# Performance work log

Measured on AMD Instinct MI355X. Metric: run time of the kernel, lower is better.

## Reference

```python
import jax, jax.numpy as jnp
import numpy as np

NZ = 1024       # opts.nz (== NH so layer-0 input weights stack with other layers)
NH = 1024       # opts.nh
NSTATE = 64     # opts.n_state
NLAYERS = 4
MAX_PRIM_LEN = 100
T = MAX_PRIM_LEN + 1   # max_unroll=True runs exactly max_prim_len+1 steps
P_BIAS = 1.0           # opts.dec_p_bias


def setup_inputs() -> dict:
    key = jax.random.key(0)
    ks = jax.random.split(key, 9)
    s_ih = 1.0 / np.sqrt(NH)
    u = lambda k, shape: jax.random.uniform(k, shape, jnp.float32, -s_ih, s_ih)
    return {
        "z": jax.random.normal(ks[0], (1, NZ), jnp.float32),
        # torch LSTM params, gate order (i, f, g, o); layer0 input dim == NZ == NH
        "Wih": u(ks[1], (NLAYERS, 4 * NH, NH)),
        "Whh": u(ks[2], (NLAYERS, 4 * NH, NH)),
        "bih": u(ks[3], (NLAYERS, 4 * NH)),
        "bhh": u(ks[4], (NLAYERS, 4 * NH)),
        "Ws": u(ks[5], (NSTATE, NH)),
        "bs": u(ks[6], (NSTATE,)),
        "Wp": u(ks[7], (2, NH)),
        "bp": u(ks[8], (2,)),
    }


def reference(z, Wih, Whh, bih, bhh, Ws, bs, Wp, bp):
    z0 = z.reshape(-1)  # (NZ,)
    zeros = jnp.zeros_like(z0)

    def step(carry, i):
        h, c = carry                      # each (NLAYERS, NH)
        x = jnp.where(i == 0, z0, zeros)  # input is z at t=0, zeros after
        hs, cs = [], []
        inp = x
        for l in range(NLAYERS):
            gates = Wih[l] @ inp + bih[l] + Whh[l] @ h[l] + bhh[l]
            gi, gf, gg, go = jnp.split(gates, 4)
            cl = jax.nn.sigmoid(gf) * c[l] + jax.nn.sigmoid(gi) * jnp.tanh(gg)
            hl = jax.nn.sigmoid(go) * jnp.tanh(cl)
            hs.append(hl)
            cs.append(cl)
            inp = hl
        o = inp                            # top-layer output, (NH,)
        s = Ws @ o + bs                    # state head, (NSTATE,)
        logits = (Wp @ o + bp).at[0].add(P_BIAS)
        p = jax.nn.softmax(logits)         # (2,)
        last = i == T - 1                  # torch: t > max_prim_len -> force [0,1]
        p = jnp.where(last, jnp.array([0.0, 1.0], p.dtype), p)
        samp = jnp.where(last, 1, 0).astype(jnp.int64)  # max_unroll forces 0 until last
        return (jnp.stack(hs), jnp.stack(cs)), (s, p, samp)

    h0 = jnp.zeros((NLAYERS, NH), z.dtype)
    _, (states, probs, samples) = jax.lax.scan(step, (h0, h0), jnp.arange(T))
    return states[:, None, :], probs[:, None, :], samples[:, None]
```

## Files before the change

### kernel.cpp

```cpp
#include <hip/hip_runtime.h>


#define TT    101
#define NBLK  256
#define NHEAD 65
#define NTH   512
#define NREP  8
#define SLAB_U32 512

#define HB16_BYTES (4 * TT * NREP * SLAB_U32 * 4)

#define OUT_PROBS 6464
#define OUT_SAMP  6666

typedef _Float16 h2 __attribute__((ext_vector_type(2)));

__device__ __forceinline__ h2 mkh2(float a, float b) {
    h2 r; r.x = (_Float16)a; r.y = (_Float16)b; return r;
}

#if __has_builtin(__builtin_amdgcn_fdot2)
__device__ __forceinline__ float fdot2(h2 a, h2 b, float c) {
    return __builtin_amdgcn_fdot2(a, b, c, false);
}
#else
__device__ __forceinline__ float fdot2(h2 a, h2 b, float c) {
    return fmaf((float)a.x, (float)b.x, fmaf((float)a.y, (float)b.y, c));
}
#endif

__device__ __forceinline__ uint4 load16_bypass(const uint4* p) {
    uint4 r;
    asm volatile("global_load_dwordx4 %0, %1, off sc0 sc1\n\ts_waitcnt vmcnt(0)"
                 : "=v"(r) : "v"(p) : "memory");
    return r;
}
__device__ __forceinline__ void store4_bypass(unsigned* p, unsigned v) {
    asm volatile("global_store_dword %0, %1, off sc0 sc1" :: "v"(p), "v"(v) : "memory");
}

__device__ __forceinline__ uint4 poll16(const uint4* p) {
    uint4 r = load16_bypass(p);
    while (r.x == 0xFFFFFFFFu || r.y == 0xFFFFFFFFu ||
           r.z == 0xFFFFFFFFu || r.w == 0xFFFFFFFFu) {
        __builtin_amdgcn_s_sleep(1);
        r = load16_bypass(p);
    }
    return r;
}

__device__ __forceinline__ float2 unpack(unsigned u) {
    h2 p = __builtin_bit_cast(h2, u);
    return make_float2((float)p.x, (float)p.y);
}

__global__ __launch_bounds__(NTH, 2) void lstm_kernel(
    const float* __restrict__ z,
    const float* __restrict__ Wih, const float* __restrict__ Whh,
    const float* __restrict__ bih, const float* __restrict__ bhh,
    const float* __restrict__ Ws,  const float* __restrict__ bs,
    const float* __restrict__ Wp,  const float* __restrict__ bp,
    unsigned* __restrict__ hb16, float* __restrict__ out)
{
    const int tid  = threadIdx.x;
    const int wv   = tid >> 6;
    const int lane = tid & 63;

    if (blockIdx.x >= NBLK) {
        if (wv != 0) return;
        const int hb  = blockIdx.x - NBLK;
        const int rep = hb & (NREP - 1);
        if (hb < 64) {
            float wr[16];
            #pragma unroll
            for (int k = 0; k < 16; ++k) wr[k] = Ws[(hb << 10) + (lane << 4) + k];
            const float bsv = bs[hb];
            for (int th = 0; th < TT; ++th) {
                const uint4* slab = (const uint4*)(hb16 + (size_t)((3 * TT + th) * NREP + rep) * SLAB_U32);
                const uint4 r0 = poll16(slab + 2 * lane);
                const uint4 r1 = poll16(slab + 2 * lane + 1);
                const unsigned u8[8] = {r0.x, r0.y, r0.z, r0.w, r1.x, r1.y, r1.z, r1.w};
                float a = 0.f;
                #pragma unroll
                for (int j = 0; j < 8; ++j) {
                    const float2 p = unpack(u8[j]);
                    a = fmaf(wr[2 * j], p.x, a);
                    a = fmaf(wr[2 * j + 1], p.y, a);
                }
                #pragma unroll
                for (int off = 1; off < 64; off <<= 1) a += __shfl_xor(a, off);
                if (lane == 0) out[th * 64 + hb] = a + bsv;
            }
        } else {
            float w0[16], w1[16];
            #pragma unroll
            for (int k = 0; k < 16; ++k) {
                w0[k] = Wp[(lane << 4) + k];
                w1[k] = Wp[1024 + (lane << 4) + k];
            }
            const float bp0 = bp[0], bp1 = bp[1];
            for (int th = 0; th < TT; ++th) {
                const uint4* slab = (const uint4*)(hb16 + (size_t)((3 * TT + th) * NREP + rep) * SLAB_U32);
                const uint4 r0 = poll16(slab + 2 * lane);
                const uint4 r1 = poll16(slab + 2 * lane + 1);
                const unsigned u8[8] = {r0.x, r0.y, r0.z, r0.w, r1.x, r1.y, r1.z, r1.w};
                float a0 = 0.f, a1 = 0.f;
                #pragma unroll
                for (int j = 0; j < 8; ++j) {
                    const float2 p = unpack(u8[j]);
                    a0 = fmaf(w0[2 * j], p.x, a0); a0 = fmaf(w0[2 * j + 1], p.y, a0);
                    a1 = fmaf(w1[2 * j], p.x, a1); a1 = fmaf(w1[2 * j + 1], p.y, a1);
                }
                #pragma unroll
                for (int off = 1; off < 64; off <<= 1) { a0 += __shfl_xor(a0, off); a1 += __shfl_xor(a1, off); }
                if (lane == 0) {
                    float p0, p1;
                    if (th == TT - 1) { p0 = 0.f; p1 = 1.f; }
                    else {
                        const float l0 = a0 + bp0 + 1.0f;
                        const float l1 = a1 + bp1;
                        const float m  = fmaxf(l0, l1);
                        const float e0 = expf(l0 - m), e1 = expf(l1 - m);
                        const float inv = 1.f / (e0 + e1);
                        p0 = e0 * inv; p1 = e1 * inv;
                    }
                    out[OUT_PROBS + 2 * th]     = p0;
                    out[OUT_PROBS + 2 * th + 1] = p1;
                    out[OUT_SAMP + th] = (th == TT - 1) ? 1.0f : 0.0f;
                }
            }
        }
        return;
    }

    const int l   = blockIdx.x >> 6;
    const int gb  = blockIdx.x & 63;
    const int uA  = (gb << 4) + (wv << 1);
    const int rep = gb & (NREP - 1);

    __shared__ __align__(16) h2 vh[1024];

    h2 w[8][16];
    #pragma unroll
    for (int r = 0; r < 8; ++r) {
        const int u = (r < 4) ? uA : (uA + 1);
        const int g = r & 3;
        const size_t row = ((size_t)((l << 12) + (g << 10) + u)) << 10;
        #pragma unroll
        for (int k = 0; k < 8; ++k) {
            const float2 fh = *(const float2*)(Whh + row + (size_t)(((k << 6) + lane) << 1));
            w[r][k] = mkh2(fh.x, fh.y);
            const float2 fi = *(const float2*)(Wih + row + (size_t)(((k << 6) + lane) << 1));
            w[r][8 + k] = mkh2(fi.x, fi.y);
        }
    }

    float bA[4], bB[4];
    #pragma unroll
    for (int g = 0; g < 4; ++g) {
        const int iA = (l << 12) + (g << 10) + uA;
        bA[g] = bih[iA] + bhh[iA];
        bB[g] = bih[iA + 1] + bhh[iA + 1];
    }

    float cst = 0.f;

    #pragma unroll 1
    for (int t = 0; t < TT; ++t) {
        const bool full = (l > 0) || (t == 0);

        if (tid < 128) {
            if (t == 0) {
                *(uint4*)&vh[tid << 2] = make_uint4(0, 0, 0, 0);
            } else {
                const uint4* slab = (const uint4*)(hb16 + (size_t)((l * TT + (t - 1)) * NREP + rep) * SLAB_U32);
                *(uint4*)&vh[tid << 2] = poll16(slab + tid);
            }
        } else if (tid < 256) {
            const int j = tid - 128;
            if (l > 0) {
                const uint4* slab = (const uint4*)(hb16 + (size_t)(((l - 1) * TT + t) * NREP + rep) * SLAB_U32);
                *(uint4*)&vh[512 + (j << 2)] = poll16(slab + j);
            } else if (t == 0) {
                const float4 f0 = *(const float4*)(z + (j << 3));
                const float4 f1 = *(const float4*)(z + (j << 3) + 4);
                h2 tmp[4] = {mkh2(f0.x, f0.y), mkh2(f0.z, f0.w),
                             mkh2(f1.x, f1.y), mkh2(f1.z, f1.w)};
                *(uint4*)&vh[512 + (j << 2)] = *(uint4*)tmp;
            }
        }
        __syncthreads();

        float acc[8] = {0.f, 0.f, 0.f, 0.f, 0.f, 0.f, 0.f, 0.f};
        #pragma unroll
        for (int k = 0; k < 8; ++k) {
            const h2 v2 = vh[(k << 6) + lane];
            #pragma unroll
            for (int r = 0; r < 8; ++r) acc[r] = fdot2(w[r][k], v2, acc[r]);
        }
        if (full) {
            #pragma unroll
            for (int k = 0; k < 8; ++k) {
                const h2 v2 = vh[512 + (k << 6) + lane];
                #pragma unroll
                for (int r = 0; r < 8; ++r) acc[r] = fdot2(w[r][8 + k], v2, acc[r]);
            }
        }
        #pragma unroll
        for (int off = 1; off < 64; off <<= 1) {
            #pragma unroll
            for (int r = 0; r < 8; ++r) acc[r] += __shfl_xor(acc[r], off);
        }

        float hv = 0.f;
        if (lane < 2) {
            float s0, s1, s2, s3;
            if (lane == 0) { s0 = acc[0] + bA[0]; s1 = acc[1] + bA[1]; s2 = acc[2] + bA[2]; s3 = acc[3] + bA[3]; }
            else           { s0 = acc[4] + bB[0]; s1 = acc[5] + bB[1]; s2 = acc[6] + bB[2]; s3 = acc[7] + bB[3]; }
            const float si = 1.f / (1.f + expf(-s0));
            const float sf = 1.f / (1.f + expf(-s1));
            const float so = 1.f / (1.f + expf(-s3));
            cst = fmaf(sf, cst, si * tanhf(s2));
            hv  = so * tanhf(cst);
        }
        const float hB = __shfl(hv, 1);
        if (lane == 0) {
            const unsigned packed = __builtin_bit_cast(unsigned, mkh2(hv, hB));
            unsigned* base = hb16 + (size_t)(l * TT + t) * NREP * SLAB_U32 + (gb << 3) + wv;
            #pragma unroll
            for (int r = 0; r < NREP; ++r) store4_bypass(base + r * SLAB_U32, packed);
        }
        __syncthreads();
    }
}

extern "C" void kernel_launch(void* const* d_in, const int* in_sizes, int n_in,
                              void* d_out, int out_size, void* d_ws, size_t ws_size,
                              hipStream_t stream)
{
    const float* z   = (const float*)d_in[0];
    const float* Wih = (const float*)d_in[1];
    const float* Whh = (const float*)d_in[2];
    const float* bih = (const float*)d_in[3];
    const float* bhh = (const float*)d_in[4];
    const float* Ws  = (const float*)d_in[5];
    const float* bs  = (const float*)d_in[6];
    const float* Wp  = (const float*)d_in[7];
    const float* bp  = (const float*)d_in[8];
    float* out = (float*)d_out;

    unsigned* hb16 = (unsigned*)d_ws;

    hipMemsetAsync(hb16, 0xFF, HB16_BYTES, stream);
    lstm_kernel<<<NBLK + NHEAD, NTH, 0, stream>>>(z, Wih, Whh, bih, bhh,
                                                  Ws, bs, Wp, bp, hb16, out);
}
```

Baseline: 566.1 us.

## Fold output heads into LSTM blocks, use DPP reductions and batched slab stores

Removes the 65 separate head blocks. The state and probability head dot products now run inside wave 6 of existing LSTM blocks, opportunistically polling the top-layer slabs a few steps behind and draining any remainder after the main loop. Wave reductions switch from shuffle-xor to DPP row operations with a readlane, and every lane computes the gate nonlinearities. The 8 hidden-state replicas are written by one wave through an LDS staging buffer instead of 8 serial stores from lane 0 of each wave. Slab replica selection is staggered per wave, and weights load as float4. The fused heads may add work to the critical path of the host blocks.

Measured after the change: 512.4 us. 9.5% less time.

```diff
diff --git a/kernel.cpp b/kernel.cpp
--- a/kernel.cpp
+++ b/kernel.cpp
@@ -3,21 +3,23 @@
 
 #define TT    101
 #define NBLK  256
-#define NHEAD 65
 #define NTH   512
 #define NREP  8
 #define SLAB_U32 512
-
 #define HB16_BYTES (4 * TT * NREP * SLAB_U32 * 4)
-
 #define OUT_PROBS 6464
 #define OUT_SAMP  6666
+#define SENT 0xFFFFFFFFu
 
 typedef _Float16 h2 __attribute__((ext_vector_type(2)));
 
 __device__ __forceinline__ h2 mkh2(float a, float b) {
     h2 r; r.x = (_Float16)a; r.y = (_Float16)b; return r;
 }
+__device__ __forceinline__ unsigned pack2(float a, float b) {
+    return __builtin_bit_cast(unsigned, mkh2(a, b));
+}
+__device__ __forceinline__ h2 as_h2(unsigned u) { return __builtin_bit_cast(h2, u); }
 
 #if __has_builtin(__builtin_amdgcn_fdot2)
 __device__ __forceinline__ float fdot2(h2 a, h2 b, float c) {
@@ -38,21 +40,33 @@
 __device__ __forceinline__ void store4_bypass(unsigned* p, unsigned v) {
     asm volatile("global_store_dword %0, %1, off sc0 sc1" :: "v"(p), "v"(v) : "memory");
 }
-
 __device__ __forceinline__ uint4 poll16(const uint4* p) {
     uint4 r = load16_bypass(p);
-    while (r.x == 0xFFFFFFFFu || r.y == 0xFFFFFFFFu ||
-           r.z == 0xFFFFFFFFu || r.w == 0xFFFFFFFFu) {
+    while (r.x == SENT || r.y == SENT || r.z == SENT || r.w == SENT) {
         __builtin_amdgcn_s_sleep(1);
         r = load16_bypass(p);
     }
     return r;
 }
 
-__device__ __forceinline__ float2 unpack(unsigned u) {
-    h2 p = __builtin_bit_cast(h2, u);
-    return make_float2((float)p.x, (float)p.y);
-}
+__device__ __forceinline__ float wave_sum(float x) {
+    int v;
+    v = __builtin_amdgcn_update_dpp(0, __builtin_bit_cast(int, x), 0x111, 0xf, 0xf, false);
+    x += __builtin_bit_cast(float, v);
+    v = __builtin_amdgcn_update_dpp(0, __builtin_bit_cast(int, x), 0x112, 0xf, 0xf, false);
+    x += __builtin_bit_cast(float, v);
+    v = __builtin_amdgcn_update_dpp(0, __builtin_bit_cast(int, x), 0x114, 0xf, 0xe, false);
+    x += __builtin_bit_cast(float, v);
+    v = __builtin_amdgcn_update_dpp(0, __builtin_bit_cast(int, x), 0x118, 0xf, 0xc, false);
+    x += __builtin_bit_cast(float, v);
+    v = __builtin_amdgcn_update_dpp(0, __builtin_bit_cast(int, x), 0x142, 0xa, 0xf, false);
+    x += __builtin_bit_cast(float, v);
+    v = __builtin_amdgcn_update_dpp(0, __builtin_bit_cast(int, x), 0x143, 0xc, 0xf, false);
+    x += __builtin_bit_cast(float, v);
+    return __builtin_bit_cast(float, __builtin_amdgcn_readlane(__builtin_bit_cast(int, x), 63));
+}
+
+__device__ __forceinline__ float sigm(float x) { return 1.f / (1.f + expf(-x)); }
 
 __global__ __launch_bounds__(NTH, 2) void lstm_kernel(
     const float* __restrict__ z,
@@ -65,60 +79,208 @@
     const int tid  = threadIdx.x;
     const int wv   = tid >> 6;
     const int lane = tid & 63;
-
-    if (blockIdx.x >= NBLK) {
-        if (wv != 0) return;
-        const int hb  = blockIdx.x - NBLK;
-        const int rep = hb & (NREP - 1);
-        if (hb < 64) {
-            float wr[16];
+    const int l    = blockIdx.x >> 6;
+    const int gb   = blockIdx.x & 63;
+    const int uA   = (gb << 4) + (wv << 1);
+
+    __shared__ __align__(16) uint4 vh4[256];
+    __shared__ unsigned hout[8];
+
+    h2 w[8][16];
+    #pragma unroll
+    for (int r = 0; r < 8; ++r) {
+        const int u = uA + (r >> 2);
+        const int g = r & 3;
+        const size_t row = ((size_t)((l << 12) + (g << 10) + u)) << 10;
+        const float4* pa = (const float4*)(Whh + row + (lane << 3));
+        const float4* pb = (const float4*)(Whh + row + 512 + (lane << 3));
+        const float4* pc = (const float4*)(Wih + row + (lane << 3));
+        const float4* pd = (const float4*)(Wih + row + 512 + (lane << 3));
+        float4 f;
+        f = pa[0]; w[r][0]  = mkh2(f.x, f.y); w[r][1]  = mkh2(f.z, f.w);
+        f = pa[1]; w[r][2]  = mkh2(f.x, f.y); w[r][3]  = mkh2(f.z, f.w);
+        f = pb[0]; w[r][4]  = mkh2(f.x, f.y); w[r][5]  = mkh2(f.z, f.w);
+        f = pb[1]; w[r][6]  = mkh2(f.x, f.y); w[r][7]  = mkh2(f.z, f.w);
+        f = pc[0]; w[r][8]  = mkh2(f.x, f.y); w[r][9]  = mkh2(f.z, f.w);
+        f = pc[1]; w[r][10] = mkh2(f.x, f.y); w[r][11] = mkh2(f.z, f.w);
+        f = pd[0]; w[r][12] = mkh2(f.x, f.y); w[r][13] = mkh2(f.z, f.w);
+        f = pd[1]; w[r][14] = mkh2(f.x, f.y); w[r][15] = mkh2(f.z, f.w);
+    }
+
+    float bA[4], bB[4];
+    #pragma unroll
+    for (int g = 0; g < 4; ++g) {
+        const int iA = (l << 12) + (g << 10) + uA;
+        bA[g] = bih[iA] + bhh[iA];
+        bB[g] = bih[iA + 1] + bhh[iA + 1];
+    }
+
+    const bool role_states = (l == 0 && wv == 6);
+    const bool role_probs  = (l == 1 && gb == 0 && wv == 6);
+    float hw0[16], hw1[16], hb0 = 0.f, hb1 = 0.f;
+    if (role_states) {
+        #pragma unroll
+        for (int k = 0; k < 16; ++k) hw0[k] = Ws[(gb << 10) + (lane << 4) + k];
+        hb0 = bs[gb];
+    } else if (role_probs) {
+        #pragma unroll
+        for (int k = 0; k < 16; ++k) {
+            hw0[k] = Wp[(lane << 4) + k];
+            hw1[k] = Wp[1024 + (lane << 4) + k];
+        }
+        hb0 = bp[0]; hb1 = bp[1];
+    }
+    int th = 0;
+
+    float cstA = 0.f, cstB = 0.f;
+
+    #pragma unroll 1
+    for (int t = 0; t < TT; ++t) {
+        const bool full = (l > 0) || (t == 0);
+        const int rep = (gb + wv) & (NREP - 1);
+
+        if (wv < 2) {
+            const int c = (wv << 6) + lane;
+            if (t == 0) vh4[c] = make_uint4(0, 0, 0, 0);
+            else {
+                const uint4* slab = (const uint4*)(hb16 + (size_t)((l * TT + t - 1) * NREP + rep) * SLAB_U32);
+                vh4[c] = poll16(slab + c);
+            }
+        } else if (wv < 4) {
+            const int c = ((wv - 2) << 6) + lane;
+            if (l > 0) {
+                const uint4* slab = (const uint4*)(hb16 + (size_t)(((l - 1) * TT + t) * NREP + rep) * SLAB_U32);
+                vh4[128 + c] = poll16(slab + c);
+            } else if (t == 0) {
+                const float4 f0 = *(const float4*)(z + (c << 3));
+                const float4 f1 = *(const float4*)(z + (c << 3) + 4);
+                vh4[128 + c] = make_uint4(pack2(f0.x, f0.y), pack2(f0.z, f0.w),
+                                          pack2(f1.x, f1.y), pack2(f1.z, f1.w));
+            }
+        }
+        __syncthreads();
+
+        float acc[8] = {0.f, 0.f, 0.f, 0.f, 0.f, 0.f, 0.f, 0.f};
+        {
+            const uint4 A1 = vh4[lane];
+            const uint4 A2 = vh4[64 + lane];
+            const unsigned a8[8] = {A1.x, A1.y, A1.z, A1.w, A2.x, A2.y, A2.z, A2.w};
             #pragma unroll
-            for (int k = 0; k < 16; ++k) wr[k] = Ws[(hb << 10) + (lane << 4) + k];
-            const float bsv = bs[hb];
-            for (int th = 0; th < TT; ++th) {
-                const uint4* slab = (const uint4*)(hb16 + (size_t)((3 * TT + th) * NREP + rep) * SLAB_U32);
-                const uint4 r0 = poll16(slab + 2 * lane);
-                const uint4 r1 = poll16(slab + 2 * lane + 1);
+            for (int k = 0; k < 8; ++k) {
+                const h2 v2 = as_h2(a8[k]);
+                #pragma unroll
+                for (int r = 0; r < 8; ++r) acc[r] = fdot2(w[r][k], v2, acc[r]);
+            }
+            if (full) {
+                const uint4 B1 = vh4[128 + lane];
+                const uint4 B2 = vh4[192 + lane];
+                const unsigned b8[8] = {B1.x, B1.y, B1.z, B1.w, B2.x, B2.y, B2.z, B2.w};
+                #pragma unroll
+                for (int k = 0; k < 8; ++k) {
+                    const h2 v2 = as_h2(b8[k]);
+                    #pragma unroll
+                    for (int r = 0; r < 8; ++r) acc[r] = fdot2(w[r][8 + k], v2, acc[r]);
+                }
+            }
+        }
+
+        float tot[8];
+        #pragma unroll
+        for (int r = 0; r < 8; ++r) tot[r] = wave_sum(acc[r]);
+
+        cstA = fmaf(sigm(tot[1] + bA[1]), cstA, sigm(tot[0] + bA[0]) * tanhf(tot[2] + bA[2]));
+        cstB = fmaf(sigm(tot[5] + bB[1]), cstB, sigm(tot[4] + bB[0]) * tanhf(tot[6] + bB[2]));
+        const float hA = sigm(tot[3] + bA[3]) * tanhf(cstA);
+        const float hB = sigm(tot[7] + bB[3]) * tanhf(cstB);
+        if (lane == 0) hout[wv] = pack2(hA, hB);
+        __syncthreads();
+
+        if (wv == 7) {
+            const unsigned val = hout[lane & 7];
+            unsigned* addr = hb16 + (size_t)(l * TT + t) * NREP * SLAB_U32
+                           + (size_t)(lane >> 3) * SLAB_U32 + (gb << 3) + (lane & 7);
+            store4_bypass(addr, val);
+        } else if ((role_states || role_probs) && th < TT && th <= t - 3) {
+            const int hrep = (gb + th) & (NREP - 1);
+            const uint4* slab3 = (const uint4*)(hb16 + (size_t)((3 * TT + th) * NREP + hrep) * SLAB_U32);
+            const uint4 r0 = load16_bypass(slab3 + (lane << 1));
+            const uint4 r1 = load16_bypass(slab3 + (lane << 1) + 1);
+            const bool ok = !(r0.x == SENT || r0.y == SENT || r0.z == SENT || r0.w == SENT ||
+                              r1.x == SENT || r1.y == SENT || r1.z == SENT || r1.w == SENT);
+            if (__ballot(ok) == ~0ull) {
                 const unsigned u8[8] = {r0.x, r0.y, r0.z, r0.w, r1.x, r1.y, r1.z, r1.w};
+                if (role_states) {
+                    float a = 0.f;
+                    #pragma unroll
+                    for (int j = 0; j < 8; ++j) {
+                        const h2 p = as_h2(u8[j]);
+                        a = fmaf(hw0[2 * j], (float)p.x, a);
+                        a = fmaf(hw0[2 * j + 1], (float)p.y, a);
+                    }
+                    const float tots = wave_sum(a);
+                    if (lane == 0) out[th * 64 + gb] = tots + hb0;
+                } else {
+                    float a0 = 0.f, a1 = 0.f;
+                    #pragma unroll
+                    for (int j = 0; j < 8; ++j) {
+                        const h2 p = as_h2(u8[j]);
+                        a0 = fmaf(hw0[2 * j], (float)p.x, a0); a0 = fmaf(hw0[2 * j + 1], (float)p.y, a0);
+                        a1 = fmaf(hw1[2 * j], (float)p.x, a1); a1 = fmaf(hw1[2 * j + 1], (float)p.y, a1);
+                    }
+                    const float t0 = wave_sum(a0), t1 = wave_sum(a1);
+                    if (lane == 0) {
+                        float p0, p1;
+                        if (th == TT - 1) { p0 = 0.f; p1 = 1.f; }
+                        else {
+                            const float l0 = t0 + hb0 + 1.0f;
+                            const float l1 = t1 + hb1;
+                            const float m  = fmaxf(l0, l1);
+                            const float e0 = expf(l0 - m), e1 = expf(l1 - m);
+                            const float inv = 1.f / (e0 + e1);
+                            p0 = e0 * inv; p1 = e1 * inv;
+                        }
+                        out[OUT_PROBS + 2 * th]     = p0;
+                        out[OUT_PROBS + 2 * th + 1] = p1;
+                        out[OUT_SAMP + th] = (th == TT - 1) ? 1.0f : 0.0f;
+                    }
+                }
+                ++th;
+            }
+        }
+    }
+
+    if (role_states || role_probs) {
+        while (th < TT) {
+            const int hrep = (gb + th) & (NREP - 1);
+            const uint4* slab3 = (const uint4*)(hb16 + (size_t)((3 * TT + th) * NREP + hrep) * SLAB_U32);
+            const uint4 r0 = poll16(slab3 + (lane << 1));
+            const uint4 r1 = poll16(slab3 + (lane << 1) + 1);
+            const unsigned u8[8] = {r0.x, r0.y, r0.z, r0.w, r1.x, r1.y, r1.z, r1.w};
+            if (role_states) {
                 float a = 0.f;
                 #pragma unroll
                 for (int j = 0; j < 8; ++j) {
-                    const float2 p = unpack(u8[j]);
-                    a = fmaf(wr[2 * j], p.x, a);
-                    a = fmaf(wr[2 * j + 1], p.y, a);
-                }
-                #pragma unroll
-                for (int off = 1; off < 64; off <<= 1) a += __shfl_xor(a, off);
-                if (lane == 0) out[th * 64 + hb] = a + bsv;
-            }
-        } else {
-            float w0[16], w1[16];
-            #pragma unroll
-            for (int k = 0; k < 16; ++k) {
-                w0[k] = Wp[(lane << 4) + k];
-                w1[k] = Wp[1024 + (lane << 4) + k];
-            }
-            const float bp0 = bp[0], bp1 = bp[1];
-            for (int th = 0; th < TT; ++th) {
-                const uint4* slab = (const uint4*)(hb16 + (size_t)((3 * TT + th) * NREP + rep) * SLAB_U32);
-                const uint4 r0 = poll16(slab + 2 * lane);
-                const uint4 r1 = poll16(slab + 2 * lane + 1);
-                const unsigned u8[8] = {r0.x, r0.y, r0.z, r0.w, r1.x, r1.y, r1.z, r1.w};
+                    const h2 p = as_h2(u8[j]);
+                    a = fmaf(hw0[2 * j], (float)p.x, a);
+                    a = fmaf(hw0[2 * j + 1], (float)p.y, a);
+                }
+                const float tots = wave_sum(a);
+                if (lane == 0) out[th * 64 + gb] = tots + hb0;
+            } else {
                 float a0 = 0.f, a1 = 0.f;
                 #pragma unroll
                 for (int j = 0; j < 8; ++j) {
-                    const float2 p = unpack(u8[j]);
-                    a0 = fmaf(w0[2 * j], p.x, a0); a0 = fmaf(w0[2 * j + 1], p.y, a0);
-                    a1 = fmaf(w1[2 * j], p.x, a1); a1 = fmaf(w1[2 * j + 1], p.y, a1);
-                }
-                #pragma unroll
-                for (int off = 1; off < 64; off <<= 1) { a0 += __shfl_xor(a0, off); a1 += __shfl_xor(a1, off); }
+                    const h2 p = as_h2(u8[j]);
+                    a0 = fmaf(hw0[2 * j], (float)p.x, a0); a0 = fmaf(hw0[2 * j + 1], (float)p.y, a0);
+                    a1 = fmaf(hw1[2 * j], (float)p.x, a1); a1 = fmaf(hw1[2 * j + 1], (float)p.y, a1);
+                }
+                const float t0 = wave_sum(a0), t1 = wave_sum(a1);
                 if (lane == 0) {
                     float p0, p1;
                     if (th == TT - 1) { p0 = 0.f; p1 = 1.f; }
                     else {
-                        const float l0 = a0 + bp0 + 1.0f;
-                        const float l1 = a1 + bp1;
+                        const float l0 = t0 + hb0 + 1.0f;
+                        const float l1 = t1 + hb1;
                         const float m  = fmaxf(l0, l1);
                         const float e0 = expf(l0 - m), e1 = expf(l1 - m);
                         const float inv = 1.f / (e0 + e1);
@@ -129,108 +291,8 @@
                     out[OUT_SAMP + th] = (th == TT - 1) ? 1.0f : 0.0f;
                 }
             }
-        }
-        return;
-    }
-
-    const int l   = blockIdx.x >> 6;
-    const int gb  = blockIdx.x & 63;
-    const int uA  = (gb << 4) + (wv << 1);
-    const int rep = gb & (NREP - 1);
-
-    __shared__ __align__(16) h2 vh[1024];
-
-    h2 w[8][16];
-    #pragma unroll
-    for (int r = 0; r < 8; ++r) {
-        const int u = (r < 4) ? uA : (uA + 1);
-        const int g = r & 3;
-        const size_t row = ((size_t)((l << 12) + (g << 10) + u)) << 10;
-        #pragma unroll
-        for (int k = 0; k < 8; ++k) {
-            const float2 fh = *(const float2*)(Whh + row + (size_t)(((k << 6) + lane) << 1));
-            w[r][k] = mkh2(fh.x, fh.y);
-            const float2 fi = *(const float2*)(Wih + row + (size_t)(((k << 6) + lane) << 1));
-            w[r][8 + k] = mkh2(fi.x, fi.y);
-        }
-    }
-
-    float bA[4], bB[4];
-    #pragma unroll
-    for (int g = 0; g < 4; ++g) {
-        const int iA = (l << 12) + (g << 10) + uA;
-        bA[g] = bih[iA] + bhh[iA];
-        bB[g] = bih[iA + 1] + bhh[iA + 1];
-    }
-
-    float cst = 0.f;
-
-    #pragma unroll 1
-    for (int t = 0; t < TT; ++t) {
-        const bool full = (l > 0) || (t == 0);
-
-        if (tid < 128) {
-            if (t == 0) {
-                *(uint4*)&vh[tid << 2] = make_uint4(0, 0, 0, 0);
-            } else {
-                const uint4* slab = (const uint4*)(hb16 + (size_t)((l * TT + (t - 1)) * NREP + rep) * SLAB_U32);
-                *(uint4*)&vh[tid << 2] = poll16(slab + tid);
-            }
-        } else if (tid < 256) {
-            const int j = tid - 128;
-            if (l > 0) {
-                const uint4* slab = (const uint4*)(hb16 + (size_t)(((l - 1) * TT + t) * NREP + rep) * SLAB_U32);
-                *(uint4*)&vh[512 + (j << 2)] = poll16(slab + j);
-            } else if (t == 0) {
-                const float4 f0 = *(const float4*)(z + (j << 3));
-                const float4 f1 = *(const float4*)(z + (j << 3) + 4);
-                h2 tmp[4] = {mkh2(f0.x, f0.y), mkh2(f0.z, f0.w),
-                             mkh2(f1.x, f1.y), mkh2(f1.z, f1.w)};
-                *(uint4*)&vh[512 + (j << 2)] = *(uint4*)tmp;
-            }
-        }
-        __syncthreads();
-
-        float acc[8] = {0.f, 0.f, 0.f, 0.f, 0.f, 0.f, 0.f, 0.f};
-        #pragma unroll
-        for (int k = 0; k < 8; ++k) {
-            const h2 v2 = vh[(k << 6) + lane];
-            #pragma unroll
-            for (int r = 0; r < 8; ++r) acc[r] = fdot2(w[r][k], v2, acc[r]);
-        }
-        if (full) {
-            #pragma unroll
-            for (int k = 0; k < 8; ++k) {
-                const h2 v2 = vh[512 + (k << 6) + lane];
-                #pragma unroll
-                for (int r = 0; r < 8; ++r) acc[r] = fdot2(w[r][8 + k], v2, acc[r]);
-            }
-        }
-        #pragma unroll
-        for (int off = 1; off < 64; off <<= 1) {
-            #pragma unroll
-            for (int r = 0; r < 8; ++r) acc[r] += __shfl_xor(acc[r], off);
-        }
-
-        float hv = 0.f;
-        if (lane < 2) {
-            float s0, s1, s2, s3;
-            if (lane == 0) { s0 = acc[0] + bA[0]; s1 = acc[1] + bA[1]; s2 = acc[2] + bA[2]; s3 = acc[3] + bA[3]; }
-            else           { s0 = acc[4] + bB[0]; s1 = acc[5] + bB[1]; s2 = acc[6] + bB[2]; s3 = acc[7] + bB[3]; }
-            const float si = 1.f / (1.f + expf(-s0));
-            const float sf = 1.f / (1.f + expf(-s1));
-            const float so = 1.f / (1.f + expf(-s3));
-            cst = fmaf(sf, cst, si * tanhf(s2));
-            hv  = so * tanhf(cst);
-        }
-        const float hB = __shfl(hv, 1);
-        if (lane == 0) {
-            const unsigned packed = __builtin_bit_cast(unsigned, mkh2(hv, hB));
-            unsigned* base = hb16 + (size_t)(l * TT + t) * NREP * SLAB_U32 + (gb << 3) + wv;
-            #pragma unroll
-            for (int r = 0; r < NREP; ++r) store4_bypass(base + r * SLAB_U32, packed);
-        }
-        __syncthreads();
+            ++th;
+        }
     }
 }
 
@@ -252,6 +314,6 @@
     unsigned* hb16 = (unsigned*)d_ws;
 
     hipMemsetAsync(hb16, 0xFF, HB16_BYTES, stream);
-    lstm_kernel<<<NBLK + NHEAD, NTH, 0, stream>>>(z, Wih, Whh, bih, bhh,
-                                                  Ws, bs, Wp, bp, hb16, out);
-}
+    lstm_kernel<<<NBLK, NTH, 0, stream>>>(z, Wih, Whh, bih, bhh,
+                                          Ws, bs, Wp, bp, hb16, out);
+}
```
